# Performance work log

Measured on AMD Instinct MI355X. Metric: run time of the kernel, lower is better.

Reference implementation:

```python
import jax, jax.numpy as jnp
import numpy as np

MESH_RESOLUTION = 0.1
ORDER = 3  # TSC interpolation


def setup_inputs() -> dict:
    key = jax.random.key(0)
    k1, k2 = jax.random.split(key)
    L = 20.0
    N, C = 100000, 8
    positions = jax.random.uniform(k1, (N, 3), dtype=jnp.float32) * L
    cell = jnp.eye(3, dtype=jnp.float32) * L
    embeddings = jax.random.normal(k2, (N, C), dtype=jnp.float32)
    return {"positions": positions, "cell": cell, "embeddings": embeddings}


def _weights_order3(dist):
    # dist: [N,3]; returns [3,N,3]
    d2 = dist * dist
    return jnp.stack([
        0.125 * (1.0 - 4.0 * dist + 4.0 * d2),
        0.25 * (3.0 - 4.0 * d2),
        0.125 * (1.0 + 4.0 * dist + 4.0 * d2),
    ])


def reference(positions, cell, embeddings):
    # Mesh setup (cubic box)
    mesh_size = float(jnp.trace(cell)) / 3.0
    n_mesh = int(2 * round(mesh_size / (2.0 * MESH_RESOLUTION)))
    spacing = mesh_size / n_mesh
    C = embeddings.shape[1]

    positions_cell = positions / spacing  # [N,3]
    # odd order: nearest-grid-point centering
    idx = jnp.round(positions_cell).astype(jnp.int32)  # [N,3]
    dist = positions_cell - idx.astype(positions_cell.dtype)  # [N,3]

    w = _weights_order3(dist)  # [3,N,3]
    offs = jnp.arange(1 - (ORDER + 1) // 2, 1 + ORDER // 2)  # [-1,0,1]
    rp = (idx[None, :, :] + offs[:, None, None]) % n_mesh  # [3,N,3]

    xs, ys, zs = jnp.meshgrid(jnp.arange(ORDER), jnp.arange(ORDER), jnp.arange(ORDER), indexing='ij')
    xs, ys, zs = xs.ravel(), ys.ravel(), zs.ravel()  # [27]

    # flat grid indices and combined weights per (corner, atom)
    flat_idx = (rp[xs, :, 0] * n_mesh + rp[ys, :, 1]) * n_mesh + rp[zs, :, 2]  # [27,N]
    wprod = w[xs, :, 0] * w[ys, :, 1] * w[zs, :, 2]  # [27,N]

    vals = wprod[:, :, None] * embeddings[None, :, :]  # [27,N,C]
    grid = jnp.zeros((n_mesh ** 3, C), dtype=positions.dtype)
    grid = grid.at[flat_idx.reshape(-1)].add(vals.reshape(-1, C))
    # -> (C, n, n, n) to match mesh.values layout
    return grid.reshape(n_mesh, n_mesh, n_mesh, C).transpose(3, 0, 1, 2)
```

## Files before the change

### kernel.cpp

```cpp
#include <hip/hip_runtime.h>
#include <math.h>


#define KColCAP 16

typedef float nfloat4 __attribute__((ext_vector_type(4)));

__device__ __forceinline__ float tsc_w(int o, float d) {
    float t = 0.5f + (float)o * d;
    return (o == 0) ? (0.75f - d * d) : (0.5f * t * t);
}

__device__ __forceinline__ float inv_spacing(const float* __restrict__ cell, int n) {
    float tr = cell[0] + cell[4] + cell[8];
    return (3.0f * (float)n) / tr;
}


__global__ __launch_bounds__(256) void fill_recs(
    const float* __restrict__ pos, const float* __restrict__ cell,
    const float* __restrict__ emb,
    int* __restrict__ counts, int* __restrict__ ovf_cnt,
    float4* __restrict__ binrec, int* __restrict__ ovf,
    int N, int n)
{
    int i = blockIdx.x * blockDim.x + threadIdx.x;
    if (i >= N) return;
    float inv_sp = inv_spacing(cell, n);
    float px = pos[3 * i + 0] * inv_sp;
    float py = pos[3 * i + 1] * inv_sp;
    float pz = pos[3 * i + 2] * inv_sp;
    int cx = (int)rintf(px); if (cx >= n) cx -= n; else if (cx < 0) cx += n;
    int cy = (int)rintf(py); if (cy >= n) cy -= n; else if (cy < 0) cy += n;
    int bin = cx * n + cy;
    int slot = atomicAdd(&counts[bin], 1);
    if (slot < KColCAP) {
        const float4* e4 = (const float4*)(emb + (size_t)i * 8);
        float4* r = binrec + (size_t)(bin * KColCAP + slot) * 3;
        r[0] = make_float4(px, py, pz, 0.0f);
        r[1] = e4[0];
        r[2] = e4[1];
    } else {
        int o = atomicAdd(ovf_cnt, 1);
        ovf[o] = i;
    }
}


__global__ __launch_bounds__(256) void gather_scatter(
    const float4* __restrict__ binrec, const int* __restrict__ counts,
    float* __restrict__ out, int n)
{
    extern __shared__ float lds[];
    const int tid = threadIdx.x;
    const int lane = tid & 63;
    const int wv = tid >> 6;
    const int y = blockIdx.x * 4 + wv;
    const int x = blockIdx.y;
    float* col = lds + wv * 8 * n;

    {
        nfloat4* c4 = (nfloat4*)col;
        const int z4 = 2 * n;
        for (int i = lane; i < z4; i += 64)
            c4[i] = (nfloat4)(0.f);
    }

    int base[9], pref[10];
    pref[0] = 0;
    #pragma unroll
    for (int j = 0; j < 9; ++j) {
        int jx = j / 3, jy = j - 3 * (j / 3);
        int xb = x + jx - 1; if (xb < 0) xb += n; else if (xb >= n) xb -= n;
        int yb = y + jy - 1; if (yb < 0) yb += n; else if (yb >= n) yb -= n;
        int bin = xb * n + yb;
        base[j] = bin * KColCAP;
        int c = counts[bin];
        c = (c < KColCAP) ? c : KColCAP;
        pref[j + 1] = pref[j] + c;
    }
    const int tot = pref[9];

    const int s  = lane / 3;
    const int zc = lane - 3 * s - 1;

    for (int q0 = 0; q0 < tot; q0 += 21) {
        const int q = q0 + s;
        if (s < 21 && q < tot) {
            int rec = base[0] + q;
            int jxv = 0, jyv = 0;
            #pragma unroll
            for (int k = 1; k < 9; ++k) {
                bool ge = (q >= pref[k]);
                int cand = base[k] + (q - pref[k]);
                rec = ge ? cand : rec;
                jxv = ge ? (k / 3) : jxv;
                jyv = ge ? (k - 3 * (k / 3)) : jyv;
            }
            const float4* rp = binrec + (size_t)rec * 3;
            float4 P  = rp[0];
            float4 e0 = rp[1];
            float4 e1 = rp[2];

            float cxf = rintf(P.x); float dx = P.x - cxf;
            float cyf = rintf(P.y); float dy = P.y - cyf;
            float czf = rintf(P.z); float dz = P.z - czf;

            float tx = 0.5f + (float)(1 - jxv) * dx;
            float wx = (jxv == 1) ? (0.75f - dx * dx) : (0.5f * tx * tx);
            float ty = 0.5f + (float)(1 - jyv) * dy;
            float wy = (jyv == 1) ? (0.75f - dy * dy) : (0.5f * ty * ty);
            float tz = 0.5f + (float)zc * dz;
            float wz = (zc == 0) ? (0.75f - dz * dz) : (0.5f * tz * tz);
            float w = wx * wy * wz;

            int cz = (int)czf; if (cz >= n) cz -= n; else if (cz < 0) cz += n;
            int z = cz + zc; if (z < 0) z += n; else if (z >= n) z -= n;

            float* p = col + z;
            atomicAdd(p + 0 * n, w * e0.x);
            atomicAdd(p + 1 * n, w * e0.y);
            atomicAdd(p + 2 * n, w * e0.z);
            atomicAdd(p + 3 * n, w * e0.w);
            atomicAdd(p + 4 * n, w * e1.x);
            atomicAdd(p + 5 * n, w * e1.y);
            atomicAdd(p + 6 * n, w * e1.z);
            atomicAdd(p + 7 * n, w * e1.w);
        }
    }
    __syncthreads();

    const int z0 = lane * 4;
    if (z0 < n) {
        const size_t n3 = (size_t)n * n * n;
        const size_t colbase = ((size_t)x * n + y) * (size_t)n + z0;
        #pragma unroll
        for (int ch = 0; ch < 8; ++ch) {
            nfloat4 v = *(const nfloat4*)(col + ch * n + z0);
            __builtin_nontemporal_store(v, (nfloat4*)(out + (size_t)ch * n3 + colbase));
        }
    }
}

__global__ __launch_bounds__(256) void deposit_overflow(
    const float* __restrict__ pos, const float* __restrict__ cell,
    const float* __restrict__ emb, const int* __restrict__ ovf_cnt,
    const int* __restrict__ ovf, float* __restrict__ out, int n)
{
    int m = *ovf_cnt;
    int i = blockIdx.x * blockDim.x + threadIdx.x;
    if (i >= m) return;
    int ai = ovf[i];
    float inv_sp = inv_spacing(cell, n);
    float p[3], d[3]; int c0[3];
    #pragma unroll
    for (int kk = 0; kk < 3; ++kk) {
        p[kk] = pos[3 * ai + kk] * inv_sp;
        c0[kk] = (int)rintf(p[kk]);
        d[kk] = p[kk] - (float)c0[kk];
    }
    float w[3][3];
    #pragma unroll
    for (int kk = 0; kk < 3; ++kk) {
        float dd = d[kk];
        w[kk][0] = tsc_w(-1, dd); w[kk][1] = tsc_w(0, dd); w[kk][2] = tsc_w(1, dd);
    }
    int W[3][3];
    #pragma unroll
    for (int kk = 0; kk < 3; ++kk)
        #pragma unroll
        for (int a = 0; a < 3; ++a) {
            int v = c0[kk] - 1 + a; if (v < 0) v += n; else if (v >= n) v -= n;
            W[kk][a] = v;
        }
    size_t n3 = (size_t)n * n * n;
    const float4* e4 = (const float4*)(emb + (size_t)ai * 8);
    float4 e0 = e4[0], e1 = e4[1];
    float e[8] = {e0.x, e0.y, e0.z, e0.w, e1.x, e1.y, e1.z, e1.w};
    for (int a = 0; a < 3; ++a)
        for (int bq = 0; bq < 3; ++bq)
            for (int cq = 0; cq < 3; ++cq) {
                float wt = w[0][a] * w[1][bq] * w[2][cq];
                size_t g = ((size_t)W[0][a] * n + W[1][bq]) * n + W[2][cq];
                #pragma unroll
                for (int ch = 0; ch < 8; ++ch)
                    atomicAdd(out + (size_t)ch * n3 + g, wt * e[ch]);
            }
}


__global__ __launch_bounds__(256) void deposit_tsc8_ilv(
    const float* __restrict__ pos,
    const float* __restrict__ cell,
    const float* __restrict__ emb,
    float* __restrict__ ws,
    int total, int n)
{
    int t = blockIdx.x * blockDim.x + threadIdx.x;
    if (t >= total) return;
    int atom = t / 27;
    int c    = t - atom * 27;
    int a    = c / 9;
    int rem  = c - a * 9;
    int b    = rem / 3;
    int cc   = rem - b * 3;

    float inv_sp = inv_spacing(cell, n);

    float px = pos[3 * atom + 0] * inv_sp;
    float py = pos[3 * atom + 1] * inv_sp;
    float pz = pos[3 * atom + 2] * inv_sp;

    int cx = (int)rintf(px);  float dx = px - (float)cx;
    int cy = (int)rintf(py);  float dy = py - (float)cy;
    int cz = (int)rintf(pz);  float dz = pz - (float)cz;

    float w = tsc_w(a - 1, dx) * tsc_w(b - 1, dy) * tsc_w(cc - 1, dz);

    int x = cx - 1 + a;  if (x < 0) x += n; else if (x >= n) x -= n;
    int y = cy - 1 + b;  if (y < 0) y += n; else if (y >= n) y -= n;
    int z = cz - 1 + cc; if (z < 0) z += n; else if (z >= n) z -= n;

    const float4* e4 = (const float4*)(emb + (size_t)atom * 8);
    float4 e0 = e4[0], e1 = e4[1];

    float* p = ws + ((size_t)((x * n + y) * n + z)) * 8;
    atomicAdd(p + 0, w * e0.x);
    atomicAdd(p + 1, w * e0.y);
    atomicAdd(p + 2, w * e0.z);
    atomicAdd(p + 3, w * e0.w);
    atomicAdd(p + 4, w * e1.x);
    atomicAdd(p + 5, w * e1.y);
    atomicAdd(p + 6, w * e1.z);
    atomicAdd(p + 7, w * e1.w);
}

__global__ __launch_bounds__(256) void transpose_ilv8(
    const float* __restrict__ ws, float* __restrict__ out, int n3)
{
    int t = blockIdx.x * blockDim.x + threadIdx.x;
    int g0 = t * 4;
    if (g0 >= n3) return;
    const float4* w4 = (const float4*)(ws + (size_t)g0 * 8);
    float4 r0 = w4[0], r1 = w4[1];
    float4 r2 = w4[2], r3 = w4[3];
    float4 r4 = w4[4], r5 = w4[5];
    float4 r6 = w4[6], r7 = w4[7];

    *(float4*)(out + (size_t)0 * n3 + g0) = make_float4(r0.x, r2.x, r4.x, r6.x);
    *(float4*)(out + (size_t)1 * n3 + g0) = make_float4(r0.y, r2.y, r4.y, r6.y);
    *(float4*)(out + (size_t)2 * n3 + g0) = make_float4(r0.z, r2.z, r4.z, r6.z);
    *(float4*)(out + (size_t)3 * n3 + g0) = make_float4(r0.w, r2.w, r4.w, r6.w);
    *(float4*)(out + (size_t)4 * n3 + g0) = make_float4(r1.x, r3.x, r5.x, r7.x);
    *(float4*)(out + (size_t)5 * n3 + g0) = make_float4(r1.y, r3.y, r5.y, r7.y);
    *(float4*)(out + (size_t)6 * n3 + g0) = make_float4(r1.z, r3.z, r5.z, r7.z);
    *(float4*)(out + (size_t)7 * n3 + g0) = make_float4(r1.w, r3.w, r5.w, r7.w);
}


__global__ __launch_bounds__(256) void deposit_tsc_gen(
    const float* __restrict__ pos,
    const float* __restrict__ cell,
    const float* __restrict__ emb,
    float* __restrict__ out,
    int N, int n, int C)
{
    int i = blockIdx.x * blockDim.x + threadIdx.x;
    if (i >= N) return;

    float inv_sp = inv_spacing(cell, n);

    float p[3], d[3];
    int c0[3];
    #pragma unroll
    for (int k = 0; k < 3; ++k) {
        p[k] = pos[3 * i + k] * inv_sp;
        c0[k] = (int)rintf(p[k]);
        d[k] = p[k] - (float)c0[k];
    }
    float w[3][3];
    #pragma unroll
    for (int k = 0; k < 3; ++k) {
        float dd = d[k], d2 = dd * dd;
        w[k][0] = 0.125f * (1.0f - 4.0f * dd + 4.0f * d2);
        w[k][1] = 0.25f  * (3.0f - 4.0f * d2);
        w[k][2] = 0.125f * (1.0f + 4.0f * dd + 4.0f * d2);
    }
    int W[3][3];
    #pragma unroll
    for (int k = 0; k < 3; ++k) {
        #pragma unroll
        for (int a = 0; a < 3; ++a) {
            int v = c0[k] - 1 + a; if (v < 0) v += n; else if (v >= n) v -= n;
            W[k][a] = v;
        }
    }
    int n3 = n * n * n;
    for (int a = 0; a < 3; ++a)
        for (int b = 0; b < 3; ++b)
            for (int cc = 0; cc < 3; ++cc) {
                float wt = w[0][a] * w[1][b] * w[2][cc];
                int g = (W[0][a] * n + W[1][b]) * n + W[2][cc];
                for (int ch = 0; ch < C; ++ch)
                    atomicAdd(out + (size_t)ch * n3 + g, wt * emb[(size_t)i * C + ch]);
            }
}

extern "C" void kernel_launch(void* const* d_in, const int* in_sizes, int n_in,
                              void* d_out, int out_size, void* d_ws, size_t ws_size,
                              hipStream_t stream) {
    const float* pos  = (const float*)d_in[0];
    const float* cell = (const float*)d_in[1];
    const float* emb  = (const float*)d_in[2];
    float* out = (float*)d_out;
    float* ws  = (float*)d_ws;

    int N = in_sizes[0] / 3;
    int C = in_sizes[2] / N;
    long long n3l = (long long)out_size / C;
    int n = (int)llroundf(cbrtf((float)n3l));
    int n3 = (int)n3l;

    int block = 256;

    {
        int nb = n * n;
        size_t lds_bytes = (size_t)4 * 8 * n * sizeof(float);
        size_t rec_off = (((size_t)nb + 4 + (size_t)N) * sizeof(int) + 15) & ~(size_t)15;
        size_t need = rec_off + (size_t)nb * KColCAP * 48;
        bool ok = (C == 8) && (n % 4 == 0) && n >= 8 && n <= 256
                  && lds_bytes <= 64 * 1024
                  && ws_size >= need
                  && ((long long)n * n * n == n3l);
        if (ok) {
            int* counts  = (int*)d_ws;
            int* ovf_cnt = counts + nb;
            int* ovf     = counts + nb + 4;
            float4* binrec = (float4*)((char*)d_ws + rec_off);

            (void)hipMemsetAsync(counts, 0, (size_t)(nb + 4) * sizeof(int), stream);
            fill_recs<<<(N + block - 1) / block, block, 0, stream>>>(
                pos, cell, emb, counts, ovf_cnt, binrec, ovf, N, n);

            dim3 grid(n / 4, n);
            gather_scatter<<<grid, block, lds_bytes, stream>>>(
                binrec, counts, out, n);

            deposit_overflow<<<(N + block - 1) / block, block, 0, stream>>>(
                pos, cell, emb, ovf_cnt, ovf, out, n);
            return;
        }
    }

    size_t need = (size_t)out_size * sizeof(float);
    if (C == 8 && ws_size >= need && (n3 % 4) == 0) {
        (void)hipMemsetAsync(d_ws, 0, need, stream);
        int total = N * 27;
        deposit_tsc8_ilv<<<(total + block - 1) / block, block, 0, stream>>>(
            pos, cell, emb, ws, total, n);
        int tthreads = n3 / 4;
        transpose_ilv8<<<(tthreads + block - 1) / block, block, 0, stream>>>(
            ws, out, n3);
    } else {
        (void)hipMemsetAsync(d_out, 0, (size_t)out_size * sizeof(float), stream);
        int grid = (N + block - 1) / block;
        deposit_tsc_gen<<<grid, block, 0, stream>>>(pos, cell, emb, out, N, n, C);
    }
}
```

Measured before the change: 145.9 us.

## Remap gather blocks across XCDs for neighbor locality, drop barrier and nontemporal stores

Flattens the gather_scatter grid to 1D and remaps block indices so each of the 8 XCDs (round-robin dispatch) gets a contiguous range of (x, y-group) columns. Neighboring columns then share bin records in the same XCD's L2. It also removes the block-wide __syncthreads, which is safe because each wavefront only touches its own LDS column, and switches the output writes from nontemporal to regular stores. Regular stores may pollute the cache, and the remap assumes the hardware dispatches blocks round-robin across XCDs.

```diff
diff --git a/kernel.cpp b/kernel.cpp
--- a/kernel.cpp
+++ b/kernel.cpp
@@ -49,14 +49,23 @@
 
 __global__ __launch_bounds__(256) void gather_scatter(
     const float4* __restrict__ binrec, const int* __restrict__ counts,
-    float* __restrict__ out, int n)
+    float* __restrict__ out, int n, int nzc)
 {
     extern __shared__ float lds[];
     const int tid = threadIdx.x;
     const int lane = tid & 63;
     const int wv = tid >> 6;
-    const int y = blockIdx.x * 4 + wv;
-    const int x = blockIdx.y;
+
+    const int nb = nzc * n;
+    const int b = blockIdx.x;
+    const int q = nb >> 3, r = nb & 7;
+    const int xcd = b & 7, idx = b >> 3;
+    const int sb = (xcd < r) ? (xcd * (q + 1) + idx)
+                             : (r * (q + 1) + (xcd - r) * q + idx);
+    const int x = sb / nzc;
+    const int ygrp = sb - x * nzc;
+    const int y = ygrp * 4 + wv;
+
     float* col = lds + wv * 8 * n;
 
     {
@@ -85,14 +94,14 @@
     const int zc = lane - 3 * s - 1;
 
     for (int q0 = 0; q0 < tot; q0 += 21) {
-        const int q = q0 + s;
-        if (s < 21 && q < tot) {
-            int rec = base[0] + q;
+        const int qq = q0 + s;
+        if (s < 21 && qq < tot) {
+            int rec = base[0] + qq;
             int jxv = 0, jyv = 0;
             #pragma unroll
             for (int k = 1; k < 9; ++k) {
-                bool ge = (q >= pref[k]);
-                int cand = base[k] + (q - pref[k]);
+                bool ge = (qq >= pref[k]);
+                int cand = base[k] + (qq - pref[k]);
                 rec = ge ? cand : rec;
                 jxv = ge ? (k / 3) : jxv;
                 jyv = ge ? (k - 3 * (k / 3)) : jyv;
@@ -128,7 +137,6 @@
             atomicAdd(p + 7 * n, w * e1.w);
         }
     }
-    __syncthreads();
 
     const int z0 = lane * 4;
     if (z0 < n) {
@@ -137,7 +145,7 @@
         #pragma unroll
         for (int ch = 0; ch < 8; ++ch) {
             nfloat4 v = *(const nfloat4*)(col + ch * n + z0);
-            __builtin_nontemporal_store(v, (nfloat4*)(out + (size_t)ch * n3 + colbase));
+            *(nfloat4*)(out + (size_t)ch * n3 + colbase) = v;
         }
     }
 }
@@ -342,9 +350,9 @@
             fill_recs<<<(N + block - 1) / block, block, 0, stream>>>(
                 pos, cell, emb, counts, ovf_cnt, binrec, ovf, N, n);
 
-            dim3 grid(n / 4, n);
-            gather_scatter<<<grid, block, lds_bytes, stream>>>(
-                binrec, counts, out, n);
+            int nzc = n / 4;
+            gather_scatter<<<nzc * n, block, lds_bytes, stream>>>(
+                binrec, counts, out, n, nzc);
 
             deposit_overflow<<<(N + block - 1) / block, block, 0, stream>>>(
                 pos, cell, emb, ovf_cnt, ovf, out, n);
```

Result: no change. 146.5 us (+0.4%).
